# Optimization experiments

Measured on AMD Instinct MI355X. Metric: run time of the kernel, lower is better.

The kernel has to match this reference:

```python
import jax, jax.numpy as jnp
import numpy as np

D_MODEL = 1024
N_HEADS = 16
HEAD_DIM = D_MODEL // N_HEADS


def setup_inputs() -> dict:
    key = jax.random.key(0)
    ks = jax.random.split(key, 5)
    B, S = 2, 2048
    x = jax.random.normal(ks[0], (B, S, D_MODEL), dtype=jnp.float32)
    # nn.Linear weights: [out_features, in_features]
    s_in = 1.0 / np.sqrt(D_MODEL)
    qkv_w = jax.random.uniform(ks[1], (3 * D_MODEL, D_MODEL), jnp.float32, -s_in, s_in)
    qkv_b = jax.random.uniform(ks[2], (3 * D_MODEL,), jnp.float32, -s_in, s_in)
    out_w = jax.random.uniform(ks[3], (D_MODEL, D_MODEL), jnp.float32, -s_in, s_in)
    out_b = jax.random.uniform(ks[4], (D_MODEL,), jnp.float32, -s_in, s_in)
    return {"x": x, "qkv_w": qkv_w, "qkv_b": qkv_b, "out_w": out_w, "out_b": out_b}


def reference(x, qkv_w, qkv_b, out_w, out_b):
    B, S, D = x.shape
    H, Hd = N_HEADS, HEAD_DIM
    scale = 1.0 / np.sqrt(Hd)
    qkv = jnp.einsum('bsd,ed->bse', x, qkv_w) + qkv_b  # [B,S,3D]
    qkv = qkv.reshape(B, S, 3, H, Hd)
    q = qkv[:, :, 0].transpose(0, 2, 1, 3)  # [B,H,S,Hd]
    k = qkv[:, :, 1].transpose(0, 2, 1, 3)
    v = qkv[:, :, 2].transpose(0, 2, 1, 3)
    scores = jnp.einsum('bhqd,bhkd->bhqk', q, k) * scale  # [B,H,S,S]
    causal = jnp.triu(jnp.ones((S, S), dtype=bool), k=1)
    scores = jnp.where(causal[None, None], -jnp.inf, scores)
    probs = jax.nn.softmax(scores, axis=-1)
    out = jnp.einsum('bhqk,bhkd->bhqd', probs, v)  # [B,H,S,Hd]
    out = out.transpose(0, 2, 1, 3).reshape(B, S, D)
    out = jnp.einsum('bsd,ed->bse', out, out_w) + out_b
    return out
```

## Files before the change

### kernel.cpp

```cpp
#include <hip/hip_runtime.h>
#include <hip/hip_bf16.h>

#define SEQ    2048
#define DMODEL 1024
#define NHEAD  16
#define HDIM   64
#define BATCH  2
#define NTOK   (BATCH * SEQ)

#define N_X   (NTOK * DMODEL)
#define N_WQ  (3 * DMODEL * DMODEL)
#define N_BQ  (3 * DMODEL)
#define N_WO  (DMODEL * DMODEL)
#define N_BO  (DMODEL)
#define N_CANON (N_X + N_WQ + N_BQ + N_WO + N_BO)

#define NEG_SENT (-1.0e30f)
#define QSCALE 0.1803368801111f

typedef __attribute__((ext_vector_type(8))) short short8;
typedef __attribute__((ext_vector_type(4))) short short4v;
typedef __attribute__((ext_vector_type(4))) float f32x4;

#define MFMA_BF16(A, B, C) __builtin_amdgcn_mfma_f32_16x16x32_bf16((A), (B), (C), 0, 0, 0)

static __device__ __forceinline__ short8 load8(const __hip_bfloat16* p) {
    return *(const short8*)p;
}

static __device__ __forceinline__ void async16(const void* g, void* l) {
    __builtin_amdgcn_global_load_lds(
        (const __attribute__((address_space(1))) unsigned int*)g,
        (__attribute__((address_space(3))) unsigned int*)l,
        16, 0, 0);
}

__global__ void detect_kernel(const unsigned short* __restrict__ w, int* flag) {
    int cnt = 0;
    for (int i = threadIdx.x; i < 512; i += 64) {
        const unsigned e = (w[i] >> 7) & 0xFF;
        if (e >= 125) cnt++;
    }
#pragma unroll
    for (int o = 32; o; o >>= 1) cnt += __shfl_down(cnt, o);
    if (threadIdx.x == 0) *flag = (cnt > 8) ? 1 : 0;
}

__global__ __launch_bounds__(256) void canon_kernel(
    const void* __restrict__ s0, const void* __restrict__ s1,
    const void* __restrict__ s2, const void* __restrict__ s3,
    const void* __restrict__ s4,
    __hip_bfloat16* __restrict__ dst, const int* __restrict__ flag)
{
    const int idx = blockIdx.x * 256 + threadIdx.x;
    if (idx >= N_CANON) return;
    const void* src;
    int off;
    if (idx < N_X)                         { src = s0; off = idx; }
    else if (idx < N_X + N_WQ)             { src = s1; off = idx - N_X; }
    else if (idx < N_X + N_WQ + N_BQ)      { src = s2; off = idx - (N_X + N_WQ); }
    else if (idx < N_X + N_WQ + N_BQ + N_WO){ src = s3; off = idx - (N_X + N_WQ + N_BQ); }
    else                                   { src = s4; off = idx - (N_X + N_WQ + N_BQ + N_WO); }
    const bool isf32 = (*flag != 0);
    const float v = isf32 ? ((const float*)src)[off]
                          : __bfloat162float(((const __hip_bfloat16*)src)[off]);
    dst[idx] = __float2bfloat16(v);
}

__global__ __launch_bounds__(256) void qkv_gemm_kernel(
    const __hip_bfloat16* __restrict__ X,
    const __hip_bfloat16* __restrict__ W,
    const __hip_bfloat16* __restrict__ bias,
    __hip_bfloat16* __restrict__ Qs,
    __hip_bfloat16* __restrict__ Kb,
    __hip_bfloat16* __restrict__ Vt)
{
    constexpr int Kd = DMODEL;
    __shared__ __align__(16) __hip_bfloat16 As[128 * 32];
    __shared__ __align__(16) __hip_bfloat16 Bs[128 * 32];

    const int tid   = threadIdx.x;
    const int lane  = tid & 63;
    const int w     = tid >> 6;
    const int mTile = blockIdx.y * 128;
    const int nTile = blockIdx.x * 128;
    const int wm    = (w >> 1) * 64;
    const int wn    = (w & 1) * 64;
    const int lm    = lane & 15;
    const int lk    = (lane >> 4) * 8;

    f32x4 acc[4][4];
#pragma unroll
    for (int i = 0; i < 4; ++i)
#pragma unroll
        for (int j = 0; j < 4; ++j)
            acc[i][j] = (f32x4){0.f, 0.f, 0.f, 0.f};

    const int r0c = tid >> 2, p0c = tid & 3;
    const int r1c = (tid + 256) >> 2, p1c = tid & 3;

    for (int k0 = 0; k0 < Kd; k0 += 32) {
        __syncthreads();
        async16(&X[(size_t)(mTile + r0c) * Kd + k0 + p0c * 8], (char*)As + tid * 16);
        async16(&X[(size_t)(mTile + r1c) * Kd + k0 + p1c * 8], (char*)As + tid * 16 + 4096);
        async16(&W[(size_t)(nTile + r0c) * Kd + k0 + p0c * 8], (char*)Bs + tid * 16);
        async16(&W[(size_t)(nTile + r1c) * Kd + k0 + p1c * 8], (char*)Bs + tid * 16 + 4096);
        __syncthreads();

        short8 a[4], b[4];
#pragma unroll
        for (int i = 0; i < 4; ++i)
            a[i] = *(const short8*)&As[(wm + i * 16 + lm) * 32 + lk];
#pragma unroll
        for (int j = 0; j < 4; ++j)
            b[j] = *(const short8*)&Bs[(wn + j * 16 + lm) * 32 + lk];
#pragma unroll
        for (int i = 0; i < 4; ++i)
#pragma unroll
            for (int j = 0; j < 4; ++j)
                acc[i][j] = MFMA_BF16(a[i], b[j], acc[i][j]);
    }

    const int r0 = (lane >> 4) * 4;
#pragma unroll
    for (int j = 0; j < 4; ++j) {
        const int n  = nTile + wn + j * 16 + lm;
        const float bv = __bfloat162float(bias[n]);
        const int c = n >> 10;
        const int h = (n >> 6) & 15;
        const int d = n & 63;
#pragma unroll
        for (int i = 0; i < 4; ++i) {
#pragma unroll
            for (int r = 0; r < 4; ++r) {
                const int m  = mTile + wm + i * 16 + r0 + r;
                const int bb = m >> 11;
                const int s  = m & (SEQ - 1);
                const int bh = bb * NHEAD + h;
                const float v = acc[i][j][r] + bv;
                if (c == 0) {
                    Qs[(size_t)(bh * SEQ + s) * HDIM + d] = __float2bfloat16(v * QSCALE);
                } else if (c == 1) {
                    Kb[(size_t)(bh * SEQ + s) * HDIM + d] = __float2bfloat16(v);
                } else {
                    Vt[(size_t)(bh * HDIM + d) * SEQ + s] = __float2bfloat16(v);
                }
            }
        }
    }
}

#define P_PITCH 72
__global__ __launch_bounds__(512, 4) void attn_kernel(
    const __hip_bfloat16* __restrict__ Qs,
    const __hip_bfloat16* __restrict__ Kb,
    const __hip_bfloat16* __restrict__ Vt,
    float* __restrict__ Opart,
    float* __restrict__ MLpart)
{
    __shared__ __align__(16) __hip_bfloat16 Kt[2][64 * 64];
    __shared__ __align__(16) __hip_bfloat16 Vs[2][64 * 64];
    __shared__ __align__(16) __hip_bfloat16 Pall[8][16 * P_PITCH];

    const int tid  = threadIdx.x;
    const int lane = tid & 63;
    const int wv   = tid >> 6;
    const int p    = blockIdx.x >> 1;
    const int kh   = blockIdx.x & 1;
    const int bh   = blockIdx.y;
    const int wgid = bh * 16 + blockIdx.x;

    const int lm  = lane & 15;
    const int q4  = lane >> 4;
    const int lk  = q4 * 8;
    const int swz = (lm & 3) << 4;

    __hip_bfloat16* P = Pall[wv];

    const __hip_bfloat16* Qbh = Qs + (size_t)bh * SEQ * HDIM;
    const __hip_bfloat16* Kbh = Kb + (size_t)bh * SEQ * HDIM;
    const __hip_bfloat16* Vbh = Vt + (size_t)bh * HDIM * SEQ;

    const int srow = tid >> 3;
    const int scb  = (tid & 7) ^ (srow & 7);

    for (int ph = 0; ph < 2; ++ph) {
        const int qb    = ph ? p : 15 - p;
        const int wbase = qb * 128 + wv * 16;
        const int nCh   = qb + 1;
        const int c0    = kh * nCh;

        short8 qa[2];
#pragma unroll
        for (int h = 0; h < 2; ++h)
            qa[h] = load8(&Qbh[(size_t)(wbase + lm) * HDIM + h * 32 + lk]);

        float m_run = NEG_SENT;
        float l_run = 0.f;
        f32x4 Oacc[4];
#pragma unroll
        for (int t = 0; t < 4; ++t) Oacc[t] = (f32x4){0.f, 0.f, 0.f, 0.f};

        int cur = 0;

        async16(&Kbh[(size_t)(c0 * 64 + srow) * HDIM + scb * 8], (char*)Kt[0] + tid * 16);
        async16(&Vbh[(size_t)srow * SEQ + c0 * 64 + scb * 8],    (char*)Vs[0] + tid * 16);

        for (int ci = 0; ci < nCh; ++ci) {
            const int k0 = (c0 + ci) * 64;

            if (ci + 1 < nCh) {
                const int k1 = k0 + 64;
                async16(&Kbh[(size_t)(k1 + srow) * HDIM + scb * 8],
                        (char*)Kt[cur ^ 1] + tid * 16);
                async16(&Vbh[(size_t)srow * SEQ + k1 + scb * 8],
                        (char*)Vs[cur ^ 1] + tid * 16);
                asm volatile("s_waitcnt vmcnt(2)" ::: "memory");
            } else {
                asm volatile("s_waitcnt vmcnt(0)" ::: "memory");
            }
            __builtin_amdgcn_s_barrier();
            __builtin_amdgcn_sched_barrier(0);

            if (k0 <= wbase + 15) {
                const __hip_bfloat16* Kc = Kt[cur];
                const __hip_bfloat16* Vc = Vs[cur];

                short8 ka[4][2];
#pragma unroll
                for (int t = 0; t < 4; ++t)
#pragma unroll
                    for (int h = 0; h < 2; ++h)
                        ka[t][h] = *(const short8*)&Kc[(t * 16 + lm) * 64 +
                                                       (((h * 4 + q4) ^ (lm & 7)) * 8)];

                f32x4 sc[4];
#pragma unroll
                for (int t = 0; t < 4; ++t) sc[t] = (f32x4){0.f, 0.f, 0.f, 0.f};
#pragma unroll
                for (int t = 0; t < 4; ++t) {
                    sc[t] = MFMA_BF16(ka[t][0], qa[0], sc[t]);
                    sc[t] = MFMA_BF16(ka[t][1], qa[1], sc[t]);
                }

                if (k0 + 63 > wbase) {
                    const int row = wbase + lm;
#pragma unroll
                    for (int t = 0; t < 4; ++t)
#pragma unroll
                        for (int r = 0; r < 4; ++r) {
                            const int key = k0 + t * 16 + q4 * 4 + r;
                            if (key > row) sc[t][r] = NEG_SENT;
                        }
                }

                float mx = sc[0][0];
#pragma unroll
                for (int t = 0; t < 4; ++t)
#pragma unroll
                    for (int r = 0; r < 4; ++r) mx = fmaxf(mx, sc[t][r]);
                mx = fmaxf(mx, __shfl_xor(mx, 16));
                mx = fmaxf(mx, __shfl_xor(mx, 32));

                if (!__all(mx <= m_run + 8.0f)) {
                    const float mn = fmaxf(m_run, mx);
                    const float alpha = exp2f(m_run - mn);
                    m_run = mn;
                    l_run *= alpha;
#pragma unroll
                    for (int r = 0; r < 4; ++r) {
                        const float av = __shfl(alpha, q4 * 4 + r);
#pragma unroll
                        for (int t = 0; t < 4; ++t) Oacc[t][r] *= av;
                    }
                }

                float s = 0.f;
#pragma unroll
                for (int t = 0; t < 4; ++t)
#pragma unroll
                    for (int r = 0; r < 4; ++r) {
                        const float pv = exp2f(sc[t][r] - m_run);
                        sc[t][r] = pv;
                        s += pv;
                    }
                s += __shfl_xor(s, 16);
                s += __shfl_xor(s, 32);
                l_run += s;

#pragma unroll
                for (int t = 0; t < 4; ++t) {
                    short4v pk;
#pragma unroll
                    for (int r = 0; r < 4; ++r)
                        pk[r] = (short)__bfloat16_as_ushort(__float2bfloat16(sc[t][r]));
                    const int col = (t * 16 + q4 * 4) ^ swz;
                    *(short4v*)&P[lm * P_PITCH + col] = pk;
                }

#pragma unroll
                for (int h = 0; h < 2; ++h) {
                    const short8 pa = *(const short8*)&P[lm * P_PITCH + ((h * 32 + lk) ^ swz)];
#pragma unroll
                    for (int t = 0; t < 4; ++t) {
                        const short8 vb = *(const short8*)&Vc[(t * 16 + lm) * 64 +
                                                              (((h * 4 + q4) ^ (lm & 7)) * 8)];
                        Oacc[t] = MFMA_BF16(pa, vb, Oacc[t]);
                    }
                }
            }

            __builtin_amdgcn_s_barrier();
            cur ^= 1;
        }

        const size_t pbase = ((size_t)wgid * 2 + ph) * 128;
#pragma unroll
        for (int t = 0; t < 4; ++t)
#pragma unroll
            for (int r = 0; r < 4; ++r)
                Opart[(pbase + wv * 16 + q4 * 4 + r) * 64 + t * 16 + lm] = Oacc[t][r];
        if (lane < 16) {
            MLpart[(pbase + wv * 16 + lane) * 2 + 0] = m_run;
            MLpart[(pbase + wv * 16 + lane) * 2 + 1] = l_run;
        }
    }
}

__global__ __launch_bounds__(256) void attn_merge_kernel(
    const float* __restrict__ Opart, const float* __restrict__ MLpart,
    __hip_bfloat16* __restrict__ O)
{
    const int idx  = blockIdx.x * 256 + threadIdx.x;
    const int d16  = idx & 3;
    const int grow = idx >> 2;
    const int bh   = grow >> 11;
    const int s    = grow & 2047;
    const int qb   = s >> 7;
    const int rin  = s & 127;
    const int p    = (qb >= 8) ? (15 - qb) : qb;
    const int ph   = (qb >= 8) ? 0 : 1;
    const size_t r0 = ((size_t)(bh * 16 + p * 2 + 0) * 2 + ph) * 128 + rin;
    const size_t r1 = ((size_t)(bh * 16 + p * 2 + 1) * 2 + ph) * 128 + rin;

    const float m1 = MLpart[r0 * 2], l1 = MLpart[r0 * 2 + 1];
    const float m2 = MLpart[r1 * 2], l2 = MLpart[r1 * 2 + 1];
    const float mm = fmaxf(m1, m2);
    const float a1 = exp2f(m1 - mm), a2 = exp2f(m2 - mm);
    const float inv = 1.0f / (a1 * l1 + a2 * l2);

    const f32x4* O1 = (const f32x4*)&Opart[r0 * 64 + d16 * 16];
    const f32x4* O2 = (const f32x4*)&Opart[r1 * 64 + d16 * 16];

    short8 out[2];
#pragma unroll
    for (int v = 0; v < 4; ++v) {
        const f32x4 x1 = O1[v], x2 = O2[v];
#pragma unroll
        for (int j = 0; j < 4; ++j)
            out[v >> 1][(v & 1) * 4 + j] = (short)__bfloat16_as_ushort(
                __float2bfloat16((a1 * x1[j] + a2 * x2[j]) * inv));
    }
    const int b = bh >> 4, hh = bh & 15;
    __hip_bfloat16* dst = &O[((size_t)b * SEQ + s) * DMODEL + hh * 64 + d16 * 16];
    ((short8*)dst)[0] = out[0];
    ((short8*)dst)[1] = out[1];
}

__global__ __launch_bounds__(256) void proj_gemm_kernel(
    const __hip_bfloat16* __restrict__ A,
    const __hip_bfloat16* __restrict__ W,
    const __hip_bfloat16* __restrict__ bias,
    void* __restrict__ outv,
    const int* __restrict__ flag)
{
    constexpr int Kd = DMODEL;
    __shared__ __align__(16) __hip_bfloat16 As[128 * 32];
    __shared__ __align__(16) __hip_bfloat16 Bs[128 * 32];

    const int tid   = threadIdx.x;
    const int lane  = tid & 63;
    const int w     = tid >> 6;
    const int mTile = blockIdx.y * 128;
    const int nTile = blockIdx.x * 128;
    const int wm    = (w >> 1) * 64;
    const int wn    = (w & 1) * 64;
    const int lm    = lane & 15;
    const int lk    = (lane >> 4) * 8;
    const bool f32out = (*flag != 0);

    f32x4 acc[4][4];
#pragma unroll
    for (int i = 0; i < 4; ++i)
#pragma unroll
        for (int j = 0; j < 4; ++j)
            acc[i][j] = (f32x4){0.f, 0.f, 0.f, 0.f};

    const int r0c = tid >> 2, p0c = tid & 3;
    const int r1c = (tid + 256) >> 2, p1c = tid & 3;

    for (int k0 = 0; k0 < Kd; k0 += 32) {
        __syncthreads();
        async16(&A[(size_t)(mTile + r0c) * Kd + k0 + p0c * 8], (char*)As + tid * 16);
        async16(&A[(size_t)(mTile + r1c) * Kd + k0 + p1c * 8], (char*)As + tid * 16 + 4096);
        async16(&W[(size_t)(nTile + r0c) * Kd + k0 + p0c * 8], (char*)Bs + tid * 16);
        async16(&W[(size_t)(nTile + r1c) * Kd + k0 + p1c * 8], (char*)Bs + tid * 16 + 4096);
        __syncthreads();

        short8 a[4], b[4];
#pragma unroll
        for (int i = 0; i < 4; ++i)
            a[i] = *(const short8*)&As[(wm + i * 16 + lm) * 32 + lk];
#pragma unroll
        for (int j = 0; j < 4; ++j)
            b[j] = *(const short8*)&Bs[(wn + j * 16 + lm) * 32 + lk];
#pragma unroll
        for (int i = 0; i < 4; ++i)
#pragma unroll
            for (int j = 0; j < 4; ++j)
                acc[i][j] = MFMA_BF16(a[i], b[j], acc[i][j]);
    }

    const int r0 = (lane >> 4) * 4;
#pragma unroll
    for (int j = 0; j < 4; ++j) {
        const int n = nTile + wn + j * 16 + lm;
        const float bv = __bfloat162float(bias[n]);
#pragma unroll
        for (int i = 0; i < 4; ++i) {
#pragma unroll
            for (int r = 0; r < 4; ++r) {
                const size_t m = mTile + wm + i * 16 + r0 + r;
                const float v = acc[i][j][r] + bv;
                if (f32out) ((float*)outv)[m * DMODEL + n] = v;
                else ((__hip_bfloat16*)outv)[m * DMODEL + n] = __float2bfloat16(v);
            }
        }
    }
}

extern "C" void kernel_launch(void* const* d_in, const int* in_sizes, int n_in,
                              void* d_out, int out_size, void* d_ws, size_t ws_size,
                              hipStream_t stream) {
    const size_t OFF_CANON = 256;
    const size_t OFF_QS = OFF_CANON + (size_t)N_CANON * 2;
    const size_t OFF_KB = OFF_QS + (size_t)NTOK * DMODEL * 2;
    const size_t OFF_VT = OFF_KB + (size_t)NTOK * DMODEL * 2;
    const size_t OFF_AO = OFF_VT + (size_t)NTOK * DMODEL * 2;
    const size_t OFF_OP = OFF_AO + (size_t)NTOK * DMODEL * 2;
    const size_t OFF_ML = OFF_OP + (size_t)512 * 2 * 128 * 64 * 4;

    char* wsb = (char*)d_ws;
    int* flag = (int*)wsb;
    __hip_bfloat16* canon = (__hip_bfloat16*)(wsb + OFF_CANON);
    __hip_bfloat16* Xc = canon;
    __hip_bfloat16* Wq = Xc + N_X;
    __hip_bfloat16* Bq = Wq + N_WQ;
    __hip_bfloat16* Wo = Bq + N_BQ;
    __hip_bfloat16* Bo = Wo + N_WO;
    __hip_bfloat16* Qs = (__hip_bfloat16*)(wsb + OFF_QS);
    __hip_bfloat16* Kb = (__hip_bfloat16*)(wsb + OFF_KB);
    __hip_bfloat16* Vt = (__hip_bfloat16*)(wsb + OFF_VT);
    __hip_bfloat16* Ao = (__hip_bfloat16*)(wsb + OFF_AO);
    float* Opart = (float*)(wsb + OFF_OP);
    float* MLpart = (float*)(wsb + OFF_ML);

    detect_kernel<<<1, 64, 0, stream>>>((const unsigned short*)d_in[1], flag);
    canon_kernel<<<(N_CANON + 255) / 256, 256, 0, stream>>>(
        d_in[0], d_in[1], d_in[2], d_in[3], d_in[4], canon, flag);

    {
        dim3 grid(3 * DMODEL / 128, NTOK / 128);
        qkv_gemm_kernel<<<grid, 256, 0, stream>>>(Xc, Wq, Bq, Qs, Kb, Vt);
    }
    {
        dim3 grid(16, BATCH * NHEAD);
        attn_kernel<<<grid, 512, 0, stream>>>(Qs, Kb, Vt, Opart, MLpart);
        attn_merge_kernel<<<(NTOK * NHEAD * 4) / 256, 256, 0, stream>>>(
            Opart, MLpart, Ao);
    }
    {
        dim3 grid(DMODEL / 128, NTOK / 128);
        proj_gemm_kernel<<<grid, 256, 0, stream>>>(Ao, Wo, Bo, d_out, flag);
    }
}
```

Before: 212.9 us.

## Double-buffer LDS tiles in QKV and projection GEMMs; vectorize V-transpose stores

Both GEMM kernels now use two LDS buffers per operand and prefetch the next K-slice with async global-to-LDS copies while MFMAs run on the current slice. Explicit vmcnt waits and raw s_barrier replace the two __syncthreads per iteration. This hides global load latency behind compute. The QKV epilogue also packs four consecutive sequence positions into one 8-byte store for the transposed V output instead of four scalar stores. The cost is doubled LDS use and reliance on hand-written waitcnt counts being correct.

```diff
diff --git a/kernel.cpp b/kernel.cpp
--- a/kernel.cpp
+++ b/kernel.cpp
@@ -76,8 +76,8 @@
     __hip_bfloat16* __restrict__ Vt)
 {
     constexpr int Kd = DMODEL;
-    __shared__ __align__(16) __hip_bfloat16 As[128 * 32];
-    __shared__ __align__(16) __hip_bfloat16 Bs[128 * 32];
+    __shared__ __align__(16) __hip_bfloat16 As[2][128 * 32];
+    __shared__ __align__(16) __hip_bfloat16 Bs[2][128 * 32];
 
     const int tid   = threadIdx.x;
     const int lane  = tid & 63;
@@ -97,28 +97,51 @@
             acc[i][j] = (f32x4){0.f, 0.f, 0.f, 0.f};
 
     const int r0c = tid >> 2, p0c = tid & 3;
-    const int r1c = (tid + 256) >> 2, p1c = tid & 3;
-
-    for (int k0 = 0; k0 < Kd; k0 += 32) {
-        __syncthreads();
-        async16(&X[(size_t)(mTile + r0c) * Kd + k0 + p0c * 8], (char*)As + tid * 16);
-        async16(&X[(size_t)(mTile + r1c) * Kd + k0 + p1c * 8], (char*)As + tid * 16 + 4096);
-        async16(&W[(size_t)(nTile + r0c) * Kd + k0 + p0c * 8], (char*)Bs + tid * 16);
-        async16(&W[(size_t)(nTile + r1c) * Kd + k0 + p1c * 8], (char*)Bs + tid * 16 + 4096);
-        __syncthreads();
-
+    const int r1c = (tid + 256) >> 2;
+
+    const __hip_bfloat16* gA0 = &X[(size_t)(mTile + r0c) * Kd + p0c * 8];
+    const __hip_bfloat16* gA1 = &X[(size_t)(mTile + r1c) * Kd + p0c * 8];
+    const __hip_bfloat16* gB0 = &W[(size_t)(nTile + r0c) * Kd + p0c * 8];
+    const __hip_bfloat16* gB1 = &W[(size_t)(nTile + r1c) * Kd + p0c * 8];
+
+    async16(gA0, (char*)As[0] + tid * 16);
+    async16(gA1, (char*)As[0] + tid * 16 + 4096);
+    async16(gB0, (char*)Bs[0] + tid * 16);
+    async16(gB1, (char*)Bs[0] + tid * 16 + 4096);
+
+    int cur = 0;
+    constexpr int NIT = Kd / 32;
+    for (int it = 0; it < NIT; ++it) {
+        if (it + 1 < NIT) {
+            const int k1 = (it + 1) * 32;
+            async16(gA0 + k1, (char*)As[cur ^ 1] + tid * 16);
+            async16(gA1 + k1, (char*)As[cur ^ 1] + tid * 16 + 4096);
+            async16(gB0 + k1, (char*)Bs[cur ^ 1] + tid * 16);
+            async16(gB1 + k1, (char*)Bs[cur ^ 1] + tid * 16 + 4096);
+            asm volatile("s_waitcnt vmcnt(4)" ::: "memory");
+        } else {
+            asm volatile("s_waitcnt vmcnt(0)" ::: "memory");
+        }
+        __builtin_amdgcn_s_barrier();
+        __builtin_amdgcn_sched_barrier(0);
+
+        const __hip_bfloat16* Ac = As[cur];
+        const __hip_bfloat16* Bc = Bs[cur];
         short8 a[4], b[4];
 #pragma unroll
         for (int i = 0; i < 4; ++i)
-            a[i] = *(const short8*)&As[(wm + i * 16 + lm) * 32 + lk];
+            a[i] = *(const short8*)&Ac[(wm + i * 16 + lm) * 32 + lk];
 #pragma unroll
         for (int j = 0; j < 4; ++j)
-            b[j] = *(const short8*)&Bs[(wn + j * 16 + lm) * 32 + lk];
+            b[j] = *(const short8*)&Bc[(wn + j * 16 + lm) * 32 + lk];
 #pragma unroll
         for (int i = 0; i < 4; ++i)
 #pragma unroll
             for (int j = 0; j < 4; ++j)
                 acc[i][j] = MFMA_BF16(a[i], b[j], acc[i][j]);
+
+        __builtin_amdgcn_s_barrier();
+        cur ^= 1;
     }
 
     const int r0 = (lane >> 4) * 4;
@@ -131,19 +154,30 @@
         const int d = n & 63;
 #pragma unroll
         for (int i = 0; i < 4; ++i) {
-#pragma unroll
-            for (int r = 0; r < 4; ++r) {
-                const int m  = mTile + wm + i * 16 + r0 + r;
-                const int bb = m >> 11;
-                const int s  = m & (SEQ - 1);
+            if (c == 2) {
+                const int m0 = mTile + wm + i * 16 + r0;
+                const int bb = m0 >> 11;
+                const int s0 = m0 & (SEQ - 1);
                 const int bh = bb * NHEAD + h;
-                const float v = acc[i][j][r] + bv;
-                if (c == 0) {
-                    Qs[(size_t)(bh * SEQ + s) * HDIM + d] = __float2bfloat16(v * QSCALE);
-                } else if (c == 1) {
-                    Kb[(size_t)(bh * SEQ + s) * HDIM + d] = __float2bfloat16(v);
-                } else {
-                    Vt[(size_t)(bh * HDIM + d) * SEQ + s] = __float2bfloat16(v);
+                short4v pk;
+#pragma unroll
+                for (int r = 0; r < 4; ++r)
+                    pk[r] = (short)__bfloat16_as_ushort(
+                        __float2bfloat16(acc[i][j][r] + bv));
+                *(short4v*)&Vt[(size_t)(bh * HDIM + d) * SEQ + s0] = pk;
+            } else {
+#pragma unroll
+                for (int r = 0; r < 4; ++r) {
+                    const int m  = mTile + wm + i * 16 + r0 + r;
+                    const int bb = m >> 11;
+                    const int s  = m & (SEQ - 1);
+                    const int bh = bb * NHEAD + h;
+                    const float v = acc[i][j][r] + bv;
+                    if (c == 0) {
+                        Qs[(size_t)(bh * SEQ + s) * HDIM + d] = __float2bfloat16(v * QSCALE);
+                    } else {
+                        Kb[(size_t)(bh * SEQ + s) * HDIM + d] = __float2bfloat16(v);
+                    }
                 }
             }
         }
@@ -375,8 +409,8 @@
     const int* __restrict__ flag)
 {
     constexpr int Kd = DMODEL;
-    __shared__ __align__(16) __hip_bfloat16 As[128 * 32];
-    __shared__ __align__(16) __hip_bfloat16 Bs[128 * 32];
+    __shared__ __align__(16) __hip_bfloat16 As[2][128 * 32];
+    __shared__ __align__(16) __hip_bfloat16 Bs[2][128 * 32];
 
     const int tid   = threadIdx.x;
     const int lane  = tid & 63;
@@ -397,28 +431,51 @@
             acc[i][j] = (f32x4){0.f, 0.f, 0.f, 0.f};
 
     const int r0c = tid >> 2, p0c = tid & 3;
-    const int r1c = (tid + 256) >> 2, p1c = tid & 3;
-
-    for (int k0 = 0; k0 < Kd; k0 += 32) {
-        __syncthreads();
-        async16(&A[(size_t)(mTile + r0c) * Kd + k0 + p0c * 8], (char*)As + tid * 16);
-        async16(&A[(size_t)(mTile + r1c) * Kd + k0 + p1c * 8], (char*)As + tid * 16 + 4096);
-        async16(&W[(size_t)(nTile + r0c) * Kd + k0 + p0c * 8], (char*)Bs + tid * 16);
-        async16(&W[(size_t)(nTile + r1c) * Kd + k0 + p1c * 8], (char*)Bs + tid * 16 + 4096);
-        __syncthreads();
-
+    const int r1c = (tid + 256) >> 2;
+
+    const __hip_bfloat16* gA0 = &A[(size_t)(mTile + r0c) * Kd + p0c * 8];
+    const __hip_bfloat16* gA1 = &A[(size_t)(mTile + r1c) * Kd + p0c * 8];
+    const __hip_bfloat16* gB0 = &W[(size_t)(nTile + r0c) * Kd + p0c * 8];
+    const __hip_bfloat16* gB1 = &W[(size_t)(nTile + r1c) * Kd + p0c * 8];
+
+    async16(gA0, (char*)As[0] + tid * 16);
+    async16(gA1, (char*)As[0] + tid * 16 + 4096);
+    async16(gB0, (char*)Bs[0] + tid * 16);
+    async16(gB1, (char*)Bs[0] + tid * 16 + 4096);
+
+    int cur = 0;
+    constexpr int NIT = Kd / 32;
+    for (int it = 0; it < NIT; ++it) {
+        if (it + 1 < NIT) {
+            const int k1 = (it + 1) * 32;
+            async16(gA0 + k1, (char*)As[cur ^ 1] + tid * 16);
+            async16(gA1 + k1, (char*)As[cur ^ 1] + tid * 16 + 4096);
+            async16(gB0 + k1, (char*)Bs[cur ^ 1] + tid * 16);
+            async16(gB1 + k1, (char*)Bs[cur ^ 1] + tid * 16 + 4096);
+            asm volatile("s_waitcnt vmcnt(4)" ::: "memory");
+        } else {
+            asm volatile("s_waitcnt vmcnt(0)" ::: "memory");
+        }
+        __builtin_amdgcn_s_barrier();
+        __builtin_amdgcn_sched_barrier(0);
+
+        const __hip_bfloat16* Ac = As[cur];
+        const __hip_bfloat16* Bc = Bs[cur];
         short8 a[4], b[4];
 #pragma unroll
         for (int i = 0; i < 4; ++i)
-            a[i] = *(const short8*)&As[(wm + i * 16 + lm) * 32 + lk];
+            a[i] = *(const short8*)&Ac[(wm + i * 16 + lm) * 32 + lk];
 #pragma unroll
         for (int j = 0; j < 4; ++j)
-            b[j] = *(const short8*)&Bs[(wn + j * 16 + lm) * 32 + lk];
+            b[j] = *(const short8*)&Bc[(wn + j * 16 + lm) * 32 + lk];
 #pragma unroll
         for (int i = 0; i < 4; ++i)
 #pragma unroll
             for (int j = 0; j < 4; ++j)
                 acc[i][j] = MFMA_BF16(a[i], b[j], acc[i][j]);
+
+        __builtin_amdgcn_s_barrier();
+        cur ^= 1;
     }
 
     const int r0 = (lane >> 4) * 4;
```

New measurement: 206.0 us. -3.2%, faster.
